# Kernel tuning notes

Measured on AMD Instinct MI355X. Metric: run time of the kernel, lower is better.

The kernel has to match this reference:

```python
import jax, jax.numpy as jnp
import numpy as np

B, DIN, HID, COMP = 16384, 1024, 512, 64

def setup_inputs() -> dict:
    key = jax.random.key(0)
    ks = jax.random.split(key, 16)
    s = lambda fan_in: 1.0 / np.sqrt(fan_in)
    return {
        "x1": jax.random.normal(ks[0], (B, DIN), jnp.float32),
        "x2": jax.random.normal(ks[1], (B, DIN), jnp.float32),
        "Wb1": jax.random.normal(ks[2], (DIN, HID), jnp.float32) * s(DIN),
        "bb1": jnp.zeros((HID,), jnp.float32),
        "Wb2": jax.random.normal(ks[3], (DIN, HID), jnp.float32) * s(DIN),
        "bb2": jnp.zeros((HID,), jnp.float32),
        "Wc1": jax.random.normal(ks[4], (HID, COMP), jnp.float32) * s(HID),
        "bc1": jnp.zeros((COMP,), jnp.float32),
        "Wc2": jax.random.normal(ks[5], (HID, COMP), jnp.float32) * s(HID),
        "bc2": jnp.zeros((COMP,), jnp.float32),
        "Wf1": jax.random.normal(ks[6], (COMP * COMP, 64), jnp.float32) * s(COMP * COMP),
        "bf1": jnp.zeros((64,), jnp.float32),
        "Wf2": jax.random.normal(ks[7], (64, 2), jnp.float32) * s(64),
        "bf2": jnp.zeros((2,), jnp.float32),
    }

def reference(x1, x2, Wb1, bb1, Wb2, bb2, Wc1, bc1, Wc2, bc2, Wf1, bf1, Wf2, bf2):
    # branch + compress: [B, DIN] -> [B, HID] -> [B, COMP]
    f1 = (jax.nn.relu(x1 @ Wb1 + bb1)) @ Wc1 + bc1  # [B, 64]
    f2 = (jax.nn.relu(x2 @ Wb2 + bb2)) @ Wc2 + bc2  # [B, 64]
    # kronecker_product(f1, f2): per-sample (f2 col) * (f1 row) -> [64,64], row-major flatten
    # element at flat index p*64 + q is f2[p] * f1[q]
    kron = jnp.einsum('bp,bq->bpq', f2, f1).reshape(f1.shape[0], -1)  # [B, 4096]
    h = kron @ Wf1 + bf1   # [B, 64]
    out = h @ Wf2 + bf2    # [B, 2]
    return out
```

## Files before the change

### kernel.cpp

```cpp
#include <hip/hip_runtime.h>

#define B_SZ 16384
#define DIN  1024
#define HID  512
#define COMP 64

typedef __bf16 bf16_t;
typedef __bf16 bf16x4 __attribute__((ext_vector_type(4)));
typedef __bf16 bf16x8 __attribute__((ext_vector_type(8)));
typedef float  f32x4  __attribute__((ext_vector_type(4)));

#define MFMA16 __builtin_amdgcn_mfma_f32_16x16x32_bf16

__device__ __forceinline__ void gl2lds16(const void* g, void* l) {
    __builtin_amdgcn_global_load_lds(
        (const __attribute__((address_space(1))) void*)g,
        (__attribute__((address_space(3))) void*)l, 16, 0, 0);
}

__device__ __forceinline__ bf16x8 cvt8(float4 a, float4 b) {
    bf16x8 o;
    o[0] = (bf16_t)a.x; o[1] = (bf16_t)a.y;
    o[2] = (bf16_t)a.z; o[3] = (bf16_t)a.w;
    o[4] = (bf16_t)b.x; o[5] = (bf16_t)b.y;
    o[6] = (bf16_t)b.z; o[7] = (bf16_t)b.w;
    return o;
}

__global__ __launch_bounds__(256) void k_prep(
    const float* __restrict__ Wb1, const float* __restrict__ Wb2,
    bf16_t* __restrict__ wbt1, bf16_t* __restrict__ wbt2,
    const float* __restrict__ Wc1, const float* __restrict__ Wc2,
    bf16_t* __restrict__ wct1, bf16_t* __restrict__ wct2,
    const float* __restrict__ Wf1, const float* __restrict__ bf1v,
    const float* __restrict__ Wf2, const float* __restrict__ bf2v,
    const float* __restrict__ bc1, const float* __restrict__ bc2,
    float* __restrict__ f1, float* __restrict__ f2,
    float* __restrict__ G, float* __restrict__ c)
{
    const int bid = blockIdx.x, tid = threadIdx.x;

    __shared__ float tile[32][33];
    const int tx = tid & 31, ty = tid >> 5;

    if (bid < 1024) {
        const int z = bid >> 9, t = bid & 511;
        const float* in  = z ? Wb2  : Wb1;
        bf16_t*      out = z ? wbt2 : wbt1;
        const int n0 = (t & 15) * 32, k0 = (t >> 4) * 32;
        #pragma unroll
        for (int i = 0; i < 4; i++)
            tile[ty + i * 8][tx] = in[(size_t)(k0 + ty + i * 8) * HID + n0 + tx];
        __syncthreads();
        #pragma unroll
        for (int i = 0; i < 4; i++)
            out[(size_t)(n0 + ty + i * 8) * DIN + k0 + tx] = (bf16_t)tile[tx][ty + i * 8];
    } else if (bid < 1088) {
        const int l = bid - 1024;
        const int z = l >> 5, t = l & 31;
        const float* in  = z ? Wc2  : Wc1;
        bf16_t*      out = z ? wct2 : wct1;
        const int n0 = (t & 1) * 32, k0 = (t >> 1) * 32;
        #pragma unroll
        for (int i = 0; i < 4; i++)
            tile[ty + i * 8][tx] = in[(size_t)(k0 + ty + i * 8) * COMP + n0 + tx];
        __syncthreads();
        #pragma unroll
        for (int i = 0; i < 4; i++)
            out[(size_t)(n0 + ty + i * 8) * HID + k0 + tx] = (bf16_t)tile[tx][ty + i * 8];
    } else if (bid < 1104) {
        const int i = (bid - 1088) * 256 + tid;
        float a0 = 0.f, a1 = 0.f;
        #pragma unroll 8
        for (int o = 0; o < 64; o++) {
            float w = Wf1[(size_t)i * 64 + o];
            a0 = fmaf(w, Wf2[o * 2 + 0], a0);
            a1 = fmaf(w, Wf2[o * 2 + 1], a1);
        }
        G[i]        = a0;
        G[4096 + i] = a1;
        if (i < 2) {
            float s = bf2v[i];
            for (int o = 0; o < 64; o++) s = fmaf(bf1v[o], Wf2[o * 2 + i], s);
            c[i] = s;
        }
    } else {
        const int l = bid - 1104;
        const int z = l >> 10;
        const float* bc = z ? bc2 : bc1;
        float*       f  = z ? f2  : f1;
        const int i = (l & 1023) * 256 + tid;
        const int c4 = (i & 15) * 4;
        float4 v = make_float4(bc[c4], bc[c4 + 1], bc[c4 + 2], bc[c4 + 3]);
        reinterpret_cast<float4*>(f)[i] = v;
    }
}

__global__ __launch_bounds__(512, 2) void k_gemm1f(
    const float* __restrict__ X1, const float* __restrict__ X2,
    const bf16_t* __restrict__ WT1, const bf16_t* __restrict__ WT2,
    const float* __restrict__ bias1, const float* __restrict__ bias2,
    const bf16_t* __restrict__ WC1, const bf16_t* __restrict__ WC2,
    float* __restrict__ F1, float* __restrict__ F2)
{
    const int bid = blockIdx.x;
    const int nid = (bid & 7) * 32 + (bid >> 3);
    const int z   = nid >> 7;
    const int nb  = (nid >> 6) & 1;
    const int mb  = nid & 63;

    const float*  X    = z ? X2    : X1;
    const bf16_t* WT   = z ? WT2   : WT1;
    const float*  bias = z ? bias2 : bias1;
    const bf16_t* WC   = z ? WC2   : WC1;
    float*        F    = z ? F2    : F1;

    const int m0 = mb * 256;
    const int n0 = nb * 256;

    __shared__ __align__(128) char smem[135168];

    const int tid  = threadIdx.x;
    const int lane = tid & 63;
    const int wave = tid >> 6;
    const int wm   = wave >> 2;
    const int wn   = wave & 3;
    const int l15  = lane & 15;
    const int g4   = lane >> 4;

    const int srow = tid >> 3;
    const int sch  = (tid & 7) ^ (srow & 7);
    const float*  gX = X  + (size_t)(m0 + srow) * DIN + sch * 8;
    const bf16_t* gB = WT + (size_t)(n0 + srow) * DIN + sch * 8;
    const int ldst = tid * 16;

    const int l7   = l15 & 7;
    const int lch0 = (g4 ^ l7) * 16;
    const int lch1 = ((4 + g4) ^ l7) * 16;
    const int abase = (wm * 64 + l15) * 128;
    const int bbase = (wn * 64 + l15) * 128;

    f32x4 acc[2][4][4] = {};
    float4 r0, r1, r2, r3;

    #pragma unroll
    for (int u = 0; u < 4; u++)
        gl2lds16(gB + (size_t)u * 64 * DIN, smem + 65536 + u * 8192 + ldst);
    r0 = *(const float4*)(gX);
    r1 = *(const float4*)(gX + 4);
    r2 = *(const float4*)(gX + (size_t)64 * DIN);
    r3 = *(const float4*)(gX + (size_t)64 * DIN + 4);
    *(bf16x8*)(smem + ldst)        = cvt8(r0, r1);
    *(bf16x8*)(smem + 8192 + ldst) = cvt8(r2, r3);
    r0 = *(const float4*)(gX + (size_t)128 * DIN);
    r1 = *(const float4*)(gX + (size_t)128 * DIN + 4);
    r2 = *(const float4*)(gX + (size_t)192 * DIN);
    r3 = *(const float4*)(gX + (size_t)192 * DIN + 4);
    *(bf16x8*)(smem + 16384 + ldst)        = cvt8(r0, r1);
    *(bf16x8*)(smem + 16384 + 8192 + ldst) = cvt8(r2, r3);
    r0 = *(const float4*)(gX + 64);
    r1 = *(const float4*)(gX + 64 + 4);
    r2 = *(const float4*)(gX + (size_t)64 * DIN + 64);
    r3 = *(const float4*)(gX + (size_t)64 * DIN + 64 + 4);
    __builtin_amdgcn_sched_barrier(0);
    asm volatile("s_waitcnt vmcnt(4) lgkmcnt(0)" ::: "memory");
    __builtin_amdgcn_s_barrier();
    __builtin_amdgcn_sched_barrier(0);

    #pragma unroll 1
    for (int kt = 0; kt < 16; ++kt) {
        const int d = kt & 1;
        const char* Ac = smem + d * 32768;
        const char* Bc = smem + 65536 + d * 32768;
        char* An = (char*)smem + (d ^ 1) * 32768;
        char* Bn = (char*)smem + 65536 + (d ^ 1) * 32768;
        const int kc1 = (kt < 15 ? kt + 1 : 15) * 64;
        const int kc2 = (kt < 14 ? kt + 2 : 15) * 64;

        bf16x8 a[4][2], b[4][2];
        #pragma unroll
        for (int mi = 0; mi < 4; mi++) {
            a[mi][0] = *(const bf16x8*)(Ac + abase + mi * 2048 + lch0);
            a[mi][1] = *(const bf16x8*)(Ac + abase + mi * 2048 + lch1);
        }
        #pragma unroll
        for (int ni = 0; ni < 4; ni++) {
            b[ni][0] = *(const bf16x8*)(Bc + bbase + ni * 2048 + lch0);
            b[ni][1] = *(const bf16x8*)(Bc + bbase + ni * 2048 + lch1);
        }
        __builtin_amdgcn_s_setprio(1);
        #pragma unroll
        for (int mi = 0; mi < 4; mi++)
            #pragma unroll
            for (int ni = 0; ni < 4; ni++) {
                acc[0][mi][ni] = MFMA16(a[mi][0], b[ni][0], acc[0][mi][ni], 0, 0, 0);
                acc[0][mi][ni] = MFMA16(a[mi][1], b[ni][1], acc[0][mi][ni], 0, 0, 0);
            }
        __builtin_amdgcn_s_setprio(0);
        __builtin_amdgcn_sched_barrier(0);

        *(bf16x8*)(An + ldst)        = cvt8(r0, r1);
        *(bf16x8*)(An + 8192 + ldst) = cvt8(r2, r3);
        __builtin_amdgcn_sched_barrier(0);
        r0 = *(const float4*)(gX + (size_t)128 * DIN + kc1);
        r1 = *(const float4*)(gX + (size_t)128 * DIN + kc1 + 4);
        r2 = *(const float4*)(gX + (size_t)192 * DIN + kc1);
        r3 = *(const float4*)(gX + (size_t)192 * DIN + kc1 + 4);
        __builtin_amdgcn_sched_barrier(0);
        gl2lds16(gB + (size_t)0 * 64 * DIN + kc1, Bn + 0 * 8192 + ldst);
        gl2lds16(gB + (size_t)1 * 64 * DIN + kc1, Bn + 1 * 8192 + ldst);
        gl2lds16(gB + (size_t)2 * 64 * DIN + kc1, Bn + 2 * 8192 + ldst);
        gl2lds16(gB + (size_t)3 * 64 * DIN + kc1, Bn + 3 * 8192 + ldst);
        __builtin_amdgcn_sched_barrier(0);

        bf16x8 a2[4][2];
        #pragma unroll
        for (int mi = 0; mi < 4; mi++) {
            a2[mi][0] = *(const bf16x8*)(Ac + 16384 + abase + mi * 2048 + lch0);
            a2[mi][1] = *(const bf16x8*)(Ac + 16384 + abase + mi * 2048 + lch1);
        }
        __builtin_amdgcn_s_setprio(1);
        #pragma unroll
        for (int mi = 0; mi < 4; mi++)
            #pragma unroll
            for (int ni = 0; ni < 4; ni++) {
                acc[1][mi][ni] = MFMA16(a2[mi][0], b[ni][0], acc[1][mi][ni], 0, 0, 0);
                acc[1][mi][ni] = MFMA16(a2[mi][1], b[ni][1], acc[1][mi][ni], 0, 0, 0);
            }
        __builtin_amdgcn_s_setprio(0);
        __builtin_amdgcn_sched_barrier(0);

        *(bf16x8*)(An + 16384 + ldst)        = cvt8(r0, r1);
        *(bf16x8*)(An + 16384 + 8192 + ldst) = cvt8(r2, r3);
        __builtin_amdgcn_sched_barrier(0);
        r0 = *(const float4*)(gX + kc2);
        r1 = *(const float4*)(gX + kc2 + 4);
        r2 = *(const float4*)(gX + (size_t)64 * DIN + kc2);
        r3 = *(const float4*)(gX + (size_t)64 * DIN + kc2 + 4);
        __builtin_amdgcn_sched_barrier(0);

        asm volatile("s_waitcnt vmcnt(4) lgkmcnt(0)" ::: "memory");
        __builtin_amdgcn_s_barrier();
        __builtin_amdgcn_sched_barrier(0);
    }

    asm volatile("s_waitcnt vmcnt(0) lgkmcnt(0)" ::: "memory");
    __builtin_amdgcn_s_barrier();

    bf16_t* Hs = (bf16_t*)smem;
    float bv[4];
    #pragma unroll
    for (int ni = 0; ni < 4; ni++)
        bv[ni] = bias[n0 + wn * 64 + ni * 16 + l15];
    #pragma unroll
    for (int ph = 0; ph < 2; ph++) {
        #pragma unroll
        for (int mi = 0; mi < 4; mi++) {
            const int lr = ph * 128 + wm * 64 + mi * 16 + g4 * 4;
            #pragma unroll
            for (int ni = 0; ni < 4; ni++) {
                const int colL = wn * 64 + ni * 16 + l15;
                #pragma unroll
                for (int r = 0; r < 4; r++) {
                    float v = fmaxf(acc[ph][mi][ni][r] + bv[ni], 0.0f);
                    Hs[(lr + r) * 264 + colL] = (bf16_t)v;
                }
            }
        }
    }
    __syncthreads();

    f32x4 acc2[2][4] = {};
    #pragma unroll
    for (int kk = 0; kk < 256; kk += 32) {
        bf16x8 af2[2];
        #pragma unroll
        for (int m2 = 0; m2 < 2; m2++)
            af2[m2] = *(const bf16x8*)(Hs + (wave * 32 + m2 * 16 + l15) * 264 + kk + g4 * 8);
        #pragma unroll
        for (int ni = 0; ni < 4; ni++) {
            bf16x8 bw = *(const bf16x8*)(&WC[(size_t)(ni * 16 + l15) * HID + n0 + kk + g4 * 8]);
            #pragma unroll
            for (int m2 = 0; m2 < 2; m2++)
                acc2[m2][ni] = MFMA16(af2[m2], bw, acc2[m2][ni], 0, 0, 0);
        }
    }
    #pragma unroll
    for (int m2 = 0; m2 < 2; m2++) {
        const int rbase = m0 + wave * 32 + m2 * 16 + g4 * 4;
        #pragma unroll
        for (int ni = 0; ni < 4; ni++) {
            const int col = ni * 16 + l15;
            #pragma unroll
            for (int r = 0; r < 4; r++)
                unsafeAtomicAdd(&F[(size_t)(rbase + r) * COMP + col], acc2[m2][ni][r]);
        }
    }
}

__global__ __launch_bounds__(256) void k_bilinear(
    const float* __restrict__ f1, const float* __restrict__ f2,
    const float* __restrict__ G, const float* __restrict__ c,
    float* __restrict__ out)
{
    __shared__ float Gs[2][4096];
    __shared__ float f1t[64][66];
    __shared__ float f2t[64][66];
    __shared__ float part[4][64];

    const int tid = threadIdx.x;
    const int s0  = blockIdx.x * 64;

    for (int i = tid; i < 2048; i += 256)
        reinterpret_cast<float4*>(&Gs[0][0])[i] =
            reinterpret_cast<const float4*>(G)[i];

    #pragma unroll
    for (int rr = 0; rr < 4; rr++) {
        const int row = (tid >> 4) + rr * 16;
        const int c4  = (tid & 15) * 4;
        float4 v1 = *reinterpret_cast<const float4*>(&f1[(size_t)(s0 + row) * 64 + c4]);
        float4 v2 = *reinterpret_cast<const float4*>(&f2[(size_t)(s0 + row) * 64 + c4]);
        f1t[c4 + 0][row] = v1.x; f1t[c4 + 1][row] = v1.y;
        f1t[c4 + 2][row] = v1.z; f1t[c4 + 3][row] = v1.w;
        f2t[c4 + 0][row] = v2.x; f2t[c4 + 1][row] = v2.y;
        f2t[c4 + 2][row] = v2.z; f2t[c4 + 3][row] = v2.w;
    }
    __syncthreads();

    const int lane = tid & 63;
    const int wv   = tid >> 6;
    const int j    = wv & 1;
    const int qh   = (wv >> 1) * 32;

    float tq[32];
    #pragma unroll
    for (int q = 0; q < 32; q++) tq[q] = 0.f;

    #pragma unroll 4
    for (int p = 0; p < 64; p++) {
        const float f2p = f2t[p][lane];
        const float* Gp = &Gs[j][p * 64 + qh];
        #pragma unroll
        for (int q4 = 0; q4 < 8; q4++) {
            float4 g = *reinterpret_cast<const float4*>(Gp + q4 * 4);
            tq[q4 * 4 + 0] = fmaf(f2p, g.x, tq[q4 * 4 + 0]);
            tq[q4 * 4 + 1] = fmaf(f2p, g.y, tq[q4 * 4 + 1]);
            tq[q4 * 4 + 2] = fmaf(f2p, g.z, tq[q4 * 4 + 2]);
            tq[q4 * 4 + 3] = fmaf(f2p, g.w, tq[q4 * 4 + 3]);
        }
    }

    float o = 0.f;
    #pragma unroll
    for (int q = 0; q < 32; q++)
        o = fmaf(f1t[qh + q][lane], tq[q], o);

    part[wv][lane] = o;
    __syncthreads();

    if (wv < 2) {
        float r = part[wv][lane] + part[wv + 2][lane] + c[wv];
        out[(size_t)(s0 + lane) * 2 + wv] = r;
    }
}

extern "C" void kernel_launch(void* const* d_in, const int* in_sizes, int n_in,
                              void* d_out, int out_size, void* d_ws, size_t ws_size,
                              hipStream_t stream)
{
    const float* x1  = (const float*)d_in[0];
    const float* x2  = (const float*)d_in[1];
    const float* Wb1 = (const float*)d_in[2];
    const float* bb1 = (const float*)d_in[3];
    const float* Wb2 = (const float*)d_in[4];
    const float* bb2 = (const float*)d_in[5];
    const float* Wc1 = (const float*)d_in[6];
    const float* bc1 = (const float*)d_in[7];
    const float* Wc2 = (const float*)d_in[8];
    const float* bc2 = (const float*)d_in[9];
    const float* Wf1 = (const float*)d_in[10];
    const float* bf1v = (const float*)d_in[11];
    const float* Wf2 = (const float*)d_in[12];
    const float* bf2v = (const float*)d_in[13];
    float* out = (float*)d_out;

    char* ws = (char*)d_ws;
    bf16_t* wbt1 = (bf16_t*)ws; ws += (size_t)HID * DIN * 2;
    bf16_t* wbt2 = (bf16_t*)ws; ws += (size_t)HID * DIN * 2;
    bf16_t* wct1 = (bf16_t*)ws; ws += (size_t)COMP * HID * 2;
    bf16_t* wct2 = (bf16_t*)ws; ws += (size_t)COMP * HID * 2;
    float*  f1   = (float*)ws;  ws += (size_t)B_SZ * COMP * 4;
    float*  f2   = (float*)ws;  ws += (size_t)B_SZ * COMP * 4;
    float*  G    = (float*)ws;  ws += (size_t)2 * 4096 * 4;
    float*  c    = (float*)ws;  ws += 256;

    k_prep<<<3152, 256, 0, stream>>>(Wb1, Wb2, wbt1, wbt2,
                                     Wc1, Wc2, wct1, wct2,
                                     Wf1, bf1v, Wf2, bf2v,
                                     bc1, bc2, f1, f2, G, c);
    k_gemm1f<<<256, 512, 0, stream>>>(x1, x2, wbt1, wbt2, bb1, bb2,
                                      wct1, wct2, f1, f2);
    k_bilinear<<<256, 256, 0, stream>>>(f1, f2, G, c, out);
}
```

Before: 215.3 us.

## Shrink GEMM1 tile to 128x128 with 256 threads and more blocks

Replaces the 256x256 tile per 512-thread block with a 128x128 tile per 256-thread block, launching 1024 blocks instead of 256 and cutting shared memory to 64KB. The pipeline is simplified to a single accumulator phase with B loads issued at loop start and the X prefetch two stages ahead. This aims to fill all CUs (256 blocks underfill a 256-CU part with 2 blocks/CU) and raise occupancy, at the cost of lower data reuse per block, more global traffic, and twice as many atomic adds into the compressed features because each block now covers only 128 hidden columns.

```diff
diff --git a/kernel.cpp b/kernel.cpp
--- a/kernel.cpp
+++ b/kernel.cpp
@@ -96,7 +96,7 @@
     }
 }
 
-__global__ __launch_bounds__(512, 2) void k_gemm1f(
+__global__ __launch_bounds__(256, 2) void k_gemm1f(
     const float* __restrict__ X1, const float* __restrict__ X2,
     const bf16_t* __restrict__ WT1, const bf16_t* __restrict__ WT2,
     const float* __restrict__ bias1, const float* __restrict__ bias2,
@@ -104,10 +104,11 @@
     float* __restrict__ F1, float* __restrict__ F2)
 {
     const int bid = blockIdx.x;
-    const int nid = (bid & 7) * 32 + (bid >> 3);
-    const int z   = nid >> 7;
-    const int nb  = (nid >> 6) & 1;
-    const int mb  = nid & 63;
+    const int nid = (bid & 7) * 128 + (bid >> 3);
+    const int z   = nid >> 9;
+    const int r9  = nid & 511;
+    const int mb  = r9 >> 2;
+    const int nb  = r9 & 3;
 
     const float*  X    = z ? X2    : X1;
     const bf16_t* WT   = z ? WT2   : WT1;
@@ -115,23 +116,23 @@
     const bf16_t* WC   = z ? WC2   : WC1;
     float*        F    = z ? F2    : F1;
 
-    const int m0 = mb * 256;
-    const int n0 = nb * 256;
-
-    __shared__ __align__(128) char smem[135168];
+    const int m0 = mb * 128;
+    const int n0 = nb * 128;
+
+    __shared__ __align__(128) char smem[65536];
 
     const int tid  = threadIdx.x;
     const int lane = tid & 63;
     const int wave = tid >> 6;
-    const int wm   = wave >> 2;
-    const int wn   = wave & 3;
+    const int wm   = wave >> 1;
+    const int wn   = wave & 1;
     const int l15  = lane & 15;
     const int g4   = lane >> 4;
 
     const int srow = tid >> 3;
-    const int sch  = (tid & 7) ^ (srow & 7);
-    const float*  gX = X  + (size_t)(m0 + srow) * DIN + sch * 8;
-    const bf16_t* gB = WT + (size_t)(n0 + srow) * DIN + sch * 8;
+    const int sc   = (tid & 7) ^ (srow & 7);
+    const float*  gX = X  + (size_t)(m0 + srow) * DIN + sc * 8;
+    const bf16_t* gB = WT + (size_t)(n0 + srow) * DIN + sc * 8;
     const int ldst = tid * 16;
 
     const int l7   = l15 & 7;
@@ -140,42 +141,44 @@
     const int abase = (wm * 64 + l15) * 128;
     const int bbase = (wn * 64 + l15) * 128;
 
-    f32x4 acc[2][4][4] = {};
-    float4 r0, r1, r2, r3;
-
-    #pragma unroll
-    for (int u = 0; u < 4; u++)
-        gl2lds16(gB + (size_t)u * 64 * DIN, smem + 65536 + u * 8192 + ldst);
-    r0 = *(const float4*)(gX);
-    r1 = *(const float4*)(gX + 4);
-    r2 = *(const float4*)(gX + (size_t)64 * DIN);
-    r3 = *(const float4*)(gX + (size_t)64 * DIN + 4);
-    *(bf16x8*)(smem + ldst)        = cvt8(r0, r1);
-    *(bf16x8*)(smem + 8192 + ldst) = cvt8(r2, r3);
-    r0 = *(const float4*)(gX + (size_t)128 * DIN);
-    r1 = *(const float4*)(gX + (size_t)128 * DIN + 4);
-    r2 = *(const float4*)(gX + (size_t)192 * DIN);
-    r3 = *(const float4*)(gX + (size_t)192 * DIN + 4);
-    *(bf16x8*)(smem + 16384 + ldst)        = cvt8(r0, r1);
-    *(bf16x8*)(smem + 16384 + 8192 + ldst) = cvt8(r2, r3);
-    r0 = *(const float4*)(gX + 64);
-    r1 = *(const float4*)(gX + 64 + 4);
-    r2 = *(const float4*)(gX + (size_t)64 * DIN + 64);
-    r3 = *(const float4*)(gX + (size_t)64 * DIN + 64 + 4);
+    f32x4  acc[4][4] = {};
+    float4 r[8];
+
+    #pragma unroll
+    for (int i = 0; i < 4; i++) {
+        r[2*i]   = *(const float4*)(gX + (size_t)i * 32 * DIN);
+        r[2*i+1] = *(const float4*)(gX + (size_t)i * 32 * DIN + 4);
+    }
+    #pragma unroll
+    for (int i = 0; i < 4; i++)
+        gl2lds16(gB + (size_t)i * 32 * DIN, smem + 32768 + i * 4096 + ldst);
+    #pragma unroll
+    for (int i = 0; i < 4; i++)
+        *(bf16x8*)(smem + i * 4096 + ldst) = cvt8(r[2*i], r[2*i+1]);
+    #pragma unroll
+    for (int i = 0; i < 4; i++) {
+        r[2*i]   = *(const float4*)(gX + (size_t)i * 32 * DIN + 64);
+        r[2*i+1] = *(const float4*)(gX + (size_t)i * 32 * DIN + 64 + 4);
+    }
     __builtin_amdgcn_sched_barrier(0);
-    asm volatile("s_waitcnt vmcnt(4) lgkmcnt(0)" ::: "memory");
+    asm volatile("s_waitcnt vmcnt(8) lgkmcnt(0)" ::: "memory");
     __builtin_amdgcn_s_barrier();
     __builtin_amdgcn_sched_barrier(0);
 
     #pragma unroll 1
     for (int kt = 0; kt < 16; ++kt) {
         const int d = kt & 1;
-        const char* Ac = smem + d * 32768;
-        const char* Bc = smem + 65536 + d * 32768;
-        char* An = (char*)smem + (d ^ 1) * 32768;
-        char* Bn = (char*)smem + 65536 + (d ^ 1) * 32768;
+        const char* Ac = smem + d * 16384;
+        const char* Bc = smem + 32768 + d * 16384;
+        char* An = (char*)smem + (d ^ 1) * 16384;
+        char* Bn = (char*)smem + 32768 + (d ^ 1) * 16384;
         const int kc1 = (kt < 15 ? kt + 1 : 15) * 64;
         const int kc2 = (kt < 14 ? kt + 2 : 15) * 64;
+
+        #pragma unroll
+        for (int i = 0; i < 4; i++)
+            gl2lds16(gB + (size_t)i * 32 * DIN + kc1, Bn + i * 4096 + ldst);
+        __builtin_amdgcn_sched_barrier(0);
 
         bf16x8 a[4][2], b[4][2];
         #pragma unroll
@@ -193,53 +196,24 @@
         for (int mi = 0; mi < 4; mi++)
             #pragma unroll
             for (int ni = 0; ni < 4; ni++) {
-                acc[0][mi][ni] = MFMA16(a[mi][0], b[ni][0], acc[0][mi][ni], 0, 0, 0);
-                acc[0][mi][ni] = MFMA16(a[mi][1], b[ni][1], acc[0][mi][ni], 0, 0, 0);
+                acc[mi][ni] = MFMA16(a[mi][0], b[ni][0], acc[mi][ni], 0, 0, 0);
+                acc[mi][ni] = MFMA16(a[mi][1], b[ni][1], acc[mi][ni], 0, 0, 0);
             }
         __builtin_amdgcn_s_setprio(0);
         __builtin_amdgcn_sched_barrier(0);
 
-        *(bf16x8*)(An + ldst)        = cvt8(r0, r1);
-        *(bf16x8*)(An + 8192 + ldst) = cvt8(r2, r3);
-        __builtin_amdgcn_sched_barrier(0);
-        r0 = *(const float4*)(gX + (size_t)128 * DIN + kc1);
-        r1 = *(const float4*)(gX + (size_t)128 * DIN + kc1 + 4);
-        r2 = *(const float4*)(gX + (size_t)192 * DIN + kc1);
-        r3 = *(const float4*)(gX + (size_t)192 * DIN + kc1 + 4);
-        __builtin_amdgcn_sched_barrier(0);
-        gl2lds16(gB + (size_t)0 * 64 * DIN + kc1, Bn + 0 * 8192 + ldst);
-        gl2lds16(gB + (size_t)1 * 64 * DIN + kc1, Bn + 1 * 8192 + ldst);
-        gl2lds16(gB + (size_t)2 * 64 * DIN + kc1, Bn + 2 * 8192 + ldst);
-        gl2lds16(gB + (size_t)3 * 64 * DIN + kc1, Bn + 3 * 8192 + ldst);
-        __builtin_amdgcn_sched_barrier(0);
-
-        bf16x8 a2[4][2];
-        #pragma unroll
-        for (int mi = 0; mi < 4; mi++) {
-            a2[mi][0] = *(const bf16x8*)(Ac + 16384 + abase + mi * 2048 + lch0);
-            a2[mi][1] = *(const bf16x8*)(Ac + 16384 + abase + mi * 2048 + lch1);
-        }
-        __builtin_amdgcn_s_setprio(1);
-        #pragma unroll
-        for (int mi = 0; mi < 4; mi++)
-            #pragma unroll
-            for (int ni = 0; ni < 4; ni++) {
-                acc[1][mi][ni] = MFMA16(a2[mi][0], b[ni][0], acc[1][mi][ni], 0, 0, 0);
-                acc[1][mi][ni] = MFMA16(a2[mi][1], b[ni][1], acc[1][mi][ni], 0, 0, 0);
-            }
-        __builtin_amdgcn_s_setprio(0);
-        __builtin_amdgcn_sched_barrier(0);
-
-        *(bf16x8*)(An + 16384 + ldst)        = cvt8(r0, r1);
-        *(bf16x8*)(An + 16384 + 8192 + ldst) = cvt8(r2, r3);
-        __builtin_amdgcn_sched_barrier(0);
-        r0 = *(const float4*)(gX + kc2);
-        r1 = *(const float4*)(gX + kc2 + 4);
-        r2 = *(const float4*)(gX + (size_t)64 * DIN + kc2);
-        r3 = *(const float4*)(gX + (size_t)64 * DIN + kc2 + 4);
-        __builtin_amdgcn_sched_barrier(0);
-
-        asm volatile("s_waitcnt vmcnt(4) lgkmcnt(0)" ::: "memory");
+        #pragma unroll
+        for (int i = 0; i < 4; i++)
+            *(bf16x8*)(An + i * 4096 + ldst) = cvt8(r[2*i], r[2*i+1]);
+        __builtin_amdgcn_sched_barrier(0);
+        #pragma unroll
+        for (int i = 0; i < 4; i++) {
+            r[2*i]   = *(const float4*)(gX + (size_t)i * 32 * DIN + kc2);
+            r[2*i+1] = *(const float4*)(gX + (size_t)i * 32 * DIN + kc2 + 4);
+        }
+        __builtin_amdgcn_sched_barrier(0);
+
+        asm volatile("s_waitcnt vmcnt(8) lgkmcnt(0)" ::: "memory");
         __builtin_amdgcn_s_barrier();
         __builtin_amdgcn_sched_barrier(0);
     }
@@ -253,18 +227,15 @@
     for (int ni = 0; ni < 4; ni++)
         bv[ni] = bias[n0 + wn * 64 + ni * 16 + l15];
     #pragma unroll
-    for (int ph = 0; ph < 2; ph++) {
-        #pragma unroll
-        for (int mi = 0; mi < 4; mi++) {
-            const int lr = ph * 128 + wm * 64 + mi * 16 + g4 * 4;
+    for (int mi = 0; mi < 4; mi++) {
+        const int lr = wm * 64 + mi * 16 + g4 * 4;
+        #pragma unroll
+        for (int ni = 0; ni < 4; ni++) {
+            const int colL = wn * 64 + ni * 16 + l15;
             #pragma unroll
-            for (int ni = 0; ni < 4; ni++) {
-                const int colL = wn * 64 + ni * 16 + l15;
-                #pragma unroll
-                for (int r = 0; r < 4; r++) {
-                    float v = fmaxf(acc[ph][mi][ni][r] + bv[ni], 0.0f);
-                    Hs[(lr + r) * 264 + colL] = (bf16_t)v;
-                }
+            for (int rr = 0; rr < 4; rr++) {
+                float v = fmaxf(acc[mi][ni][rr] + bv[ni], 0.0f);
+                Hs[(lr + rr) * 136 + colL] = (bf16_t)v;
             }
         }
     }
@@ -272,11 +243,11 @@
 
     f32x4 acc2[2][4] = {};
     #pragma unroll
-    for (int kk = 0; kk < 256; kk += 32) {
+    for (int kk = 0; kk < 128; kk += 32) {
         bf16x8 af2[2];
         #pragma unroll
         for (int m2 = 0; m2 < 2; m2++)
-            af2[m2] = *(const bf16x8*)(Hs + (wave * 32 + m2 * 16 + l15) * 264 + kk + g4 * 8);
+            af2[m2] = *(const bf16x8*)(Hs + (wave * 32 + m2 * 16 + l15) * 136 + kk + g4 * 8);
         #pragma unroll
         for (int ni = 0; ni < 4; ni++) {
             bf16x8 bw = *(const bf16x8*)(&WC[(size_t)(ni * 16 + l15) * HID + n0 + kk + g4 * 8]);
@@ -292,8 +263,8 @@
         for (int ni = 0; ni < 4; ni++) {
             const int col = ni * 16 + l15;
             #pragma unroll
-            for (int r = 0; r < 4; r++)
-                unsafeAtomicAdd(&F[(size_t)(rbase + r) * COMP + col], acc2[m2][ni][r]);
+            for (int rr = 0; rr < 4; rr++)
+                unsafeAtomicAdd(&F[(size_t)(rbase + rr) * COMP + col], acc2[m2][ni][rr]);
         }
     }
 }
@@ -399,7 +370,7 @@
                                      Wc1, Wc2, wct1, wct2,
                                      Wf1, bf1v, Wf2, bf2v,
                                      bc1, bc2, f1, f2, G, c);
-    k_gemm1f<<<256, 512, 0, stream>>>(x1, x2, wbt1, wbt2, bb1, bb2,
-                                      wct1, wct2, f1, f2);
+    k_gemm1f<<<1024, 256, 0, stream>>>(x1, x2, wbt1, wbt2, bb1, bb2,
+                                       wct1, wct2, f1, f2);
     k_bilinear<<<256, 256, 0, stream>>>(f1, f2, G, c, out);
 }
```

After: 238.8 us. 10.9% more time.
